# Kernel tuning notes

Hardware: AMD Instinct MI355X
Metric: run time of the kernel (lower is better)

## Reference

```python
import jax, jax.numpy as jnp
import numpy as np

B, N, F, K = 16384, 64, 128, 64


def setup_inputs() -> dict:
    key = jax.random.key(0)
    kx, kd = jax.random.split(key)
    x = jax.random.normal(kx, (B, F), dtype=jnp.float32)
    D = jax.random.normal(kd, (N, F, K), dtype=jnp.float32)  # per-cluster factor dictionaries
    return {"x": x, "D": D}


def reference(x, D):
    # --- assignment step (torch.no_grad in original) ---
    # Dtx[n,b,j] = sum_i D[n,i,j] * x[b,i]
    Dtx = jnp.einsum('nij,bi->nbj', D, x)                      # [N,B,K]
    # per-cluster (D^T D)^{-1}, batched inverse over the cluster axis
    DTD = jnp.einsum('nij,nik->njk', D, D)                     # [N,K,K]
    DTD_inv = jnp.linalg.inv(DTD)                              # [N,K,K]
    Cs = jnp.einsum('nbj,nkj->nbk', Dtx, DTD_inv)              # [N,B,K]
    x_hat = jnp.einsum('nij,nbj->nbi', D, Cs)                  # [N,B,F]
    # nearest-subspace assignment per sample
    label = jnp.argmin(jnp.linalg.norm(x_hat - x[None], axis=-1), axis=0)  # [B] int
    C = Cs[label, jnp.arange(x.shape[0])]                      # [B,K] gather per sample
    # --- reconstruction loss: sum_i || x[i] - D[label[i]] @ C[i] ||^2 ---
    x_rec = jnp.einsum('bik,bk->bi', D[label], C)              # grouped gather + matmul
    se_loss = jnp.sum(jnp.square(x - x_rec))
    return se_loss, label
```

## Files before the change

kernel.cpp:

```cpp
#include <hip/hip_runtime.h>
#include <hip/hip_bf16.h>

#define B_N 16384
#define TAU 0.25f
#define GS 68
#define YS 133

typedef float f32x4 __attribute__((ext_vector_type(4)));
typedef short s16x8 __attribute__((ext_vector_type(8)));

__device__ __forceinline__ void gl_lds16(const void* g, void* l) {
    __builtin_amdgcn_global_load_lds(
        (const __attribute__((address_space(1))) void*)g,
        (__attribute__((address_space(3))) void*)l, 16, 0, 0);
}

__device__ __forceinline__ unsigned short bf16_bits(float v) {
    __hip_bfloat16 h = __float2bfloat16(v);
    return *reinterpret_cast<unsigned short*>(&h);
}

__global__ __launch_bounds__(256) void prep_convert(const float* __restrict__ x,
                                                    const float* __restrict__ D,
                                                    unsigned short* __restrict__ xh,
                                                    float* __restrict__ nrm,
                                                    float* __restrict__ Qg,
                                                    unsigned short* __restrict__ Bht,
                                                    float* __restrict__ out) {
    const int t = threadIdx.x;

    if (blockIdx.x >= 64) {
        const int gid = (blockIdx.x - 64) * 256 + t;
        if (gid == 0) out[0] = 0.0f;
        const size_t base = (size_t)gid * 32;
        float s = 0.0f;
        #pragma unroll
        for (int c = 0; c < 8; ++c) {
            const f32x4 v = ((const f32x4*)(x + base))[c];
            s += v.x * v.x + v.y * v.y + v.z * v.z + v.w * v.w;
            ushort4 h;
            h.x = bf16_bits(v.x); h.y = bf16_bits(v.y);
            h.z = bf16_bits(v.z); h.w = bf16_bits(v.w);
            ((ushort4*)(xh + base))[c] = h;
        }
        s += __shfl_xor(s, 1, 64);
        s += __shfl_xor(s, 2, 64);
        if ((gid & 3) == 0) nrm[gid >> 2] = s;
        return;
    }

    __shared__ float Y[64 * YS];
    __shared__ __align__(16) float G[64 * GS + 64];
    __shared__ __align__(16) float Lti[8 * 8 * 8];
    const int n = blockIdx.x;
    const float* Dn = D + (size_t)n * 8192;

    for (int e4 = t; e4 < 2048; e4 += 256) {
        const int c = e4 >> 4, j4 = (e4 & 15) * 4;
        const f32x4 v = ((const f32x4*)Dn)[e4];
        Y[(j4 + 0) * YS + c] = v.x;
        Y[(j4 + 1) * YS + c] = v.y;
        Y[(j4 + 2) * YS + c] = v.z;
        Y[(j4 + 3) * YS + c] = v.w;
    }

    {
        const int a0 = (t & 15) * 4, b0 = (t >> 4) * 4;
        float acc[4][4] = {};
        #pragma unroll 4
        for (int i = 0; i < 128; ++i) {
            const f32x4 av = *(const f32x4*)(Dn + i * 64 + a0);
            const f32x4 bv = *(const f32x4*)(Dn + i * 64 + b0);
            const float aa[4] = {av.x, av.y, av.z, av.w};
            const float bb[4] = {bv.x, bv.y, bv.z, bv.w};
            #pragma unroll
            for (int p = 0; p < 4; ++p)
                #pragma unroll
                for (int q = 0; q < 4; ++q) acc[p][q] = fmaf(aa[p], bb[q], acc[p][q]);
        }
        #pragma unroll
        for (int p = 0; p < 4; ++p)
            #pragma unroll
            for (int q = 0; q < 4; ++q) G[(a0 + p) * GS + b0 + q] = acc[p][q];
    }
    __syncthreads();

    for (int p8 = 0; p8 < 8; ++p8) {
        const int pb = p8 * 8;
        if (t < 64) {
            const int lane = t;
            const f32x4 v0 = *(const f32x4*)&G[lane * GS + pb];
            const f32x4 v1 = *(const f32x4*)&G[lane * GS + pb + 4];
            float g[8] = {v0.x, v0.y, v0.z, v0.w, v1.x, v1.y, v1.z, v1.w};
            #pragma unroll
            for (int kk = 0; kk < 8; ++kk) {
                const int k = pb + kk;
                const float dk = __shfl(g[kk], k, 64);
                const float rinv = 1.0f / sqrtf(dk);
                const float lik = g[kk] * rinv;
                g[kk] = lik;
                if (lane == 0) G[64 * GS + k] = rinv;
                #pragma unroll
                for (int jj = kk + 1; jj < 8; ++jj) {
                    const float ljk = __shfl(lik, pb + jj, 64);
                    g[jj] -= lik * ljk;
                }
            }
            *(f32x4*)&G[lane * GS + pb]     = (f32x4){g[0], g[1], g[2], g[3]};
            *(f32x4*)&G[lane * GS + pb + 4] = (f32x4){g[4], g[5], g[6], g[7]};
        }
        __syncthreads();
        const int base = pb + 8;
        if (base < 64) {
            for (int i = base + (t >> 5); i < 64; i += 8) {
                const f32x4 Li0 = *(const f32x4*)&G[i * GS + pb];
                const f32x4 Li1 = *(const f32x4*)&G[i * GS + pb + 4];
                for (int j = base + (t & 31); j < 64; j += 32) {
                    const f32x4 Lj0 = *(const f32x4*)&G[j * GS + pb];
                    const f32x4 Lj1 = *(const f32x4*)&G[j * GS + pb + 4];
                    float s = G[i * GS + j];
                    s -= Li0.x * Lj0.x + Li0.y * Lj0.y + Li0.z * Lj0.z + Li0.w * Lj0.w;
                    s -= Li1.x * Lj1.x + Li1.y * Lj1.y + Li1.z * Lj1.z + Li1.w * Lj1.w;
                    G[i * GS + j] = s;
                }
            }
        }
        __syncthreads();
    }

    if (t < 64) {
        const int bi = t >> 3, c = t & 7;
        const int base = bi * 8;
        float m[8];
        #pragma unroll
        for (int r = 0; r < 8; ++r) {
            float s = (r == c) ? 1.0f : 0.0f;
            #pragma unroll
            for (int k = 0; k < r; ++k)
                s -= G[(base + r) * GS + base + k] * m[k];
            m[r] = s * G[64 * GS + base + r];
        }
        #pragma unroll
        for (int r = 0; r < 8; ++r) Lti[(base + r) * 8 + c] = m[r];
    }
    __syncthreads();

    if (t < 128) {
        const int c = t;
        for (int i = 0; i < 8; ++i) {
            float Tv[8];
            #pragma unroll
            for (int r = 0; r < 8; ++r) Tv[r] = Y[(i * 8 + r) * YS + c];
            for (int k = 0; k < i; ++k) {
                #pragma unroll
                for (int kk = 0; kk < 8; ++kk) {
                    const float z = Y[(k * 8 + kk) * YS + c];
                    #pragma unroll
                    for (int r = 0; r < 8; ++r)
                        Tv[r] -= G[(i * 8 + r) * GS + k * 8 + kk] * z;
                }
            }
            #pragma unroll
            for (int r = 0; r < 8; ++r) {
                float z = 0.0f;
                #pragma unroll
                for (int rp = 0; rp <= r; ++rp)
                    z += Lti[(i * 8 + r) * 8 + rp] * Tv[rp];
                Y[(i * 8 + r) * YS + c] = z;
            }
        }
    }
    __syncthreads();

    for (int e = t; e < 8192; e += 256) {
        const int j = e >> 7, i = e & 127;
        Bht[((size_t)n * 64 + j) * 128 + i] = bf16_bits(Y[j * YS + i]);
    }
    for (int e = t; e < 8192; e += 256) {
        const int i = e >> 6, j = e & 63;
        Qg[(size_t)n * 8192 + e] = Y[j * YS + i];
    }
}

__global__ __launch_bounds__(256) void gemm_scores(const unsigned short* __restrict__ xh,
                                                   const unsigned short* __restrict__ Bht,
                                                   float* __restrict__ S) {
    __shared__ unsigned short ldsA[128 * 128];
    __shared__ unsigned short ldsB[128 * 128];
    const int t = threadIdx.x, w = t >> 6, lane = t & 63;
    const int m0 = blockIdx.x * 128;
    const int nsplit = blockIdx.y;
    const int wm = w & 1, wn = w >> 1;

    {
        const int rl = lane >> 4;
        const int p  = lane & 15;
        #pragma unroll
        for (int q = 0; q < 8; ++q) {
            const int row = w * 32 + q * 4 + rl;
            const int c = p ^ (row & 15);
            gl_lds16(xh + (size_t)(m0 + row) * 128 + c * 8,
                     &ldsA[(w * 32 + q * 4) * 128]);
            gl_lds16(Bht + (size_t)(nsplit * 1024 + row) * 128 + c * 8,
                     &ldsB[(w * 32 + q * 4) * 128]);
        }
    }
    __syncthreads();

    s16x8 af[4][4];
    #pragma unroll
    for (int mt = 0; mt < 4; ++mt) {
        const int r = wm * 64 + mt * 16 + (lane & 15);
        #pragma unroll
        for (int ks = 0; ks < 4; ++ks) {
            const int p = (ks * 4 + (lane >> 4)) ^ (lane & 15);
            af[mt][ks] = *(const s16x8*)&ldsA[r * 128 + p * 8];
        }
    }

    #pragma unroll 1
    for (int it = 0; it < 8; ++it) {
        s16x8 bf[4][4];
        #pragma unroll
        for (int nt = 0; nt < 4; ++nt) {
            const int r = wn * 64 + nt * 16 + (lane & 15);
            #pragma unroll
            for (int ks = 0; ks < 4; ++ks) {
                const int p = (ks * 4 + (lane >> 4)) ^ (lane & 15);
                bf[nt][ks] = *(const s16x8*)&ldsB[r * 128 + p * 8];
            }
        }
        __syncthreads();

        if (it < 7) {
            const int rl = lane >> 4, p = lane & 15;
            #pragma unroll
            for (int q = 0; q < 8; ++q) {
                const int row = w * 32 + q * 4 + rl;
                const int c = p ^ (row & 15);
                gl_lds16(Bht + (size_t)(nsplit * 1024 + (it + 1) * 128 + row) * 128 + c * 8,
                         &ldsB[(w * 32 + q * 4) * 128]);
            }
        }

        const int nc = nsplit * 16 + it * 2 + wn;
        #pragma unroll
        for (int mt = 0; mt < 4; ++mt) {
            f32x4 acc[4];
            #pragma unroll
            for (int nt = 0; nt < 4; ++nt) acc[nt] = (f32x4){0.f, 0.f, 0.f, 0.f};
            #pragma unroll
            for (int ks = 0; ks < 4; ++ks)
                #pragma unroll
                for (int nt = 0; nt < 4; ++nt)
                    acc[nt] = __builtin_amdgcn_mfma_f32_16x16x32_bf16(
                        af[mt][ks], bf[nt][ks], acc[nt], 0, 0, 0);
            #pragma unroll
            for (int rg = 0; rg < 4; ++rg) {
                float p = 0.0f;
                #pragma unroll
                for (int nt = 0; nt < 4; ++nt) {
                    const float v = acc[nt][rg];
                    p += v * v;
                }
                p += __shfl_xor(p, 1, 64);
                p += __shfl_xor(p, 2, 64);
                p += __shfl_xor(p, 4, 64);
                p += __shfl_xor(p, 8, 64);
                if ((lane & 15) == 0) {
                    const int m = wm * 64 + mt * 16 + (lane >> 4) * 4 + rg;
                    S[(size_t)nc * B_N + m0 + m] = p;
                }
            }
        }
        __syncthreads();
    }
}

__global__ __launch_bounds__(256) void argmax_rescore(const float* __restrict__ Sa,
                                                      const float* __restrict__ nrm,
                                                      const float* __restrict__ x,
                                                      const float* __restrict__ Qg,
                                                      float* __restrict__ out) {
    __shared__ float tile[64 * 65];
    __shared__ int sflags[64];
    __shared__ int scnt;
    __shared__ float ssum;
    __shared__ float scorr[4];
    const int t = threadIdx.x, w = t >> 6, lane = t & 63;
    const int b0 = blockIdx.x * 64;
    if (t == 0) scnt = 0;

    for (int idx = t; idx < 1024; idx += 256) {
        const int n = idx >> 4, c4 = idx & 15;
        const f32x4 v = *(const f32x4*)&Sa[(size_t)n * B_N + b0 + c4 * 4];
        tile[(c4 * 4 + 0) * 65 + n] = v.x;
        tile[(c4 * 4 + 1) * 65 + n] = v.y;
        tile[(c4 * 4 + 2) * 65 + n] = v.z;
        tile[(c4 * 4 + 3) * 65 + n] = v.w;
    }
    __syncthreads();

    if (t < 64) {
        float v1 = -1e30f, v2 = -1e30f;
        int n1 = 0;
        for (int n = 0; n < 64; ++n) {
            const float v = tile[t * 65 + n];
            if (v > v1) { v2 = v1; v1 = v; n1 = n; }
            else v2 = fmaxf(v2, v);
        }
        out[1 + b0 + t] = (float)n1;
        if (v1 - v2 < TAU) { const int i = atomicAdd(&scnt, 1); sflags[i] = t; }
        float err = nrm[b0 + t] - v1;
        for (int off = 32; off; off >>= 1) err += __shfl_xor(err, off, 64);
        if (t == 0) ssum = err;
    }
    if (lane == 0) scorr[w] = 0.0f;
    __syncthreads();

    const int nf = scnt;
    float corr = 0.0f;
    for (int f = w; f < nf; f += 4) {
        const int s = sflags[f];
        const int b2 = b0 + s;
        const float v = tile[s * 65 + lane];
        float vm = v;
        for (int off = 32; off; off >>= 1) vm = fmaxf(vm, __shfl_xor(vm, off, 64));
        unsigned long long mask = __ballot((vm - v) < TAU);
        float best = -1e30f;
        int bn = 0;
        while (mask) {
            const int nn = (int)__builtin_ctzll(mask);
            mask &= mask - 1;
            const float* Qn = Qg + (size_t)nn * 8192;
            const float* xb = x + (size_t)b2 * 128;
            float d0 = 0.0f, d1 = 0.0f, d2 = 0.0f, d3 = 0.0f;
            #pragma unroll
            for (int i = 0; i < 128; i += 4) {
                d0 = fmaf(Qn[(i + 0) * 64 + lane], xb[i + 0], d0);
                d1 = fmaf(Qn[(i + 1) * 64 + lane], xb[i + 1], d1);
                d2 = fmaf(Qn[(i + 2) * 64 + lane], xb[i + 2], d2);
                d3 = fmaf(Qn[(i + 3) * 64 + lane], xb[i + 3], d3);
            }
            const float dot = (d0 + d1) + (d2 + d3);
            float sv = dot * dot;
            for (int off = 32; off; off >>= 1) sv += __shfl_xor(sv, off, 64);
            if (sv > best) { best = sv; bn = nn; }
        }
        if (lane == 0) {
            out[1 + b2] = (float)bn;
            corr += vm - best;
        }
    }
    if (lane == 0 && corr != 0.0f) scorr[w] += corr;
    __syncthreads();
    if (t == 0)
        atomicAdd(out, ssum + scorr[0] + scorr[1] + scorr[2] + scorr[3]);
}

extern "C" void kernel_launch(void* const* d_in, const int* in_sizes, int n_in,
                              void* d_out, int out_size, void* d_ws, size_t ws_size,
                              hipStream_t stream) {
    const float* x = (const float*)d_in[0];
    const float* D = (const float*)d_in[1];
    float* out = (float*)d_out;

    char* ws = (char*)d_ws;
    unsigned short* xh  = (unsigned short*)(ws);
    unsigned short* Bht = (unsigned short*)(ws + (4u << 20));
    float* Qg           = (float*)(ws + (5u << 20));
    float* Sa           = (float*)(ws + (7u << 20));
    float* nrm          = (float*)(ws + (11u << 20));

    prep_convert<<<320, 256, 0, stream>>>(x, D, xh, nrm, Qg, Bht, out);
    gemm_scores<<<dim3(128, 4), 256, 0, stream>>>(xh, Bht, Sa);
    argmax_rescore<<<256, 256, 0, stream>>>(Sa, nrm, x, Qg, out);
}
```

Measured before the change: 161.3 us.

## Fuse score GEMM with argmax and rescore, keeping scores in LDS

Merges the scoring GEMM and the argmax/rescore kernels into one kernel. Each block now covers 64 samples across all 64 clusters and keeps its score tile in shared memory that reuses the A/B staging space, so the global score array is no longer written and read back and one launch disappears. In exchange, the M tile shrinks from 128 to 64 rows and each block streams the whole Bht matrix. That halves reuse of B and roughly doubles L2 traffic for B, while the grid drops to 256 blocks.

```diff
diff --git a/kernel.cpp b/kernel.cpp
--- a/kernel.cpp
+++ b/kernel.cpp
@@ -182,70 +182,84 @@
     }
 }
 
-__global__ __launch_bounds__(256) void gemm_scores(const unsigned short* __restrict__ xh,
+__global__ __launch_bounds__(256) void gemm_argmax(const unsigned short* __restrict__ xh,
                                                    const unsigned short* __restrict__ Bht,
-                                                   float* __restrict__ S) {
-    __shared__ unsigned short ldsA[128 * 128];
-    __shared__ unsigned short ldsB[128 * 128];
+                                                   const float* __restrict__ nrm,
+                                                   const float* __restrict__ x,
+                                                   const float* __restrict__ Qg,
+                                                   float* __restrict__ out) {
+    __shared__ __align__(16) unsigned char lds_raw[49152];
+    unsigned short* ldsA = (unsigned short*)lds_raw;
+    unsigned short* ldsB = (unsigned short*)(lds_raw + 16384);
+    float* St = (float*)lds_raw;
+    __shared__ int sflags[64];
+    __shared__ int scnt;
+    __shared__ float ssum;
+    __shared__ float scorr[4];
+
     const int t = threadIdx.x, w = t >> 6, lane = t & 63;
-    const int m0 = blockIdx.x * 128;
-    const int nsplit = blockIdx.y;
+    const int b0 = blockIdx.x * 64;
     const int wm = w & 1, wn = w >> 1;
+    if (t == 0) scnt = 0;
 
     {
-        const int rl = lane >> 4;
-        const int p  = lane & 15;
+        const int rl = lane >> 4, p = lane & 15;
+        #pragma unroll
+        for (int q = 0; q < 4; ++q) {
+            const int row = w * 16 + q * 4 + rl;
+            const int c = p ^ (row & 15);
+            gl_lds16(xh + (size_t)(b0 + row) * 128 + c * 8,
+                     &ldsA[(w * 16 + q * 4) * 128]);
+        }
         #pragma unroll
         for (int q = 0; q < 8; ++q) {
             const int row = w * 32 + q * 4 + rl;
             const int c = p ^ (row & 15);
-            gl_lds16(xh + (size_t)(m0 + row) * 128 + c * 8,
-                     &ldsA[(w * 32 + q * 4) * 128]);
-            gl_lds16(Bht + (size_t)(nsplit * 1024 + row) * 128 + c * 8,
+            gl_lds16(Bht + (size_t)row * 128 + c * 8,
                      &ldsB[(w * 32 + q * 4) * 128]);
         }
     }
     __syncthreads();
 
-    s16x8 af[4][4];
+    s16x8 af[2][4];
     #pragma unroll
-    for (int mt = 0; mt < 4; ++mt) {
-        const int r = wm * 64 + mt * 16 + (lane & 15);
+    for (int mt = 0; mt < 2; ++mt) {
+        const int r = wm * 32 + mt * 16 + (lane & 15);
         #pragma unroll
         for (int ks = 0; ks < 4; ++ks) {
-            const int p = (ks * 4 + (lane >> 4)) ^ (lane & 15);
+            const int p = (ks * 4 + (lane >> 4)) ^ (r & 15);
             af[mt][ks] = *(const s16x8*)&ldsA[r * 128 + p * 8];
         }
     }
 
     #pragma unroll 1
-    for (int it = 0; it < 8; ++it) {
+    for (int it = 0; it < 32; ++it) {
         s16x8 bf[4][4];
         #pragma unroll
         for (int nt = 0; nt < 4; ++nt) {
             const int r = wn * 64 + nt * 16 + (lane & 15);
             #pragma unroll
             for (int ks = 0; ks < 4; ++ks) {
-                const int p = (ks * 4 + (lane >> 4)) ^ (lane & 15);
+                const int p = (ks * 4 + (lane >> 4)) ^ (r & 15);
                 bf[nt][ks] = *(const s16x8*)&ldsB[r * 128 + p * 8];
             }
         }
         __syncthreads();
 
-        if (it < 7) {
+        if (it < 31) {
             const int rl = lane >> 4, p = lane & 15;
             #pragma unroll
             for (int q = 0; q < 8; ++q) {
                 const int row = w * 32 + q * 4 + rl;
                 const int c = p ^ (row & 15);
-                gl_lds16(Bht + (size_t)(nsplit * 1024 + (it + 1) * 128 + row) * 128 + c * 8,
+                gl_lds16(Bht + (size_t)((it + 1) * 128 + row) * 128 + c * 8,
                          &ldsB[(w * 32 + q * 4) * 128]);
             }
         }
 
-        const int nc = nsplit * 16 + it * 2 + wn;
-        #pragma unroll
-        for (int mt = 0; mt < 4; ++mt) {
+        const int nc = it * 2 + wn;
+        #pragma unroll
+        for (int mt = 0; mt < 2; ++mt) {
             f32x4 acc[4];
             #pragma unroll
             for (int nt = 0; nt < 4; ++nt) acc[nt] = (f32x4){0.f, 0.f, 0.f, 0.f};
@@ -268,44 +282,19 @@
                 p += __shfl_xor(p, 4, 64);
                 p += __shfl_xor(p, 8, 64);
                 if ((lane & 15) == 0) {
-                    const int m = wm * 64 + mt * 16 + (lane >> 4) * 4 + rg;
-                    S[(size_t)nc * B_N + m0 + m] = p;
+                    const int m = wm * 32 + mt * 16 + (lane >> 4) * 4 + rg;
+                    St[nc * 64 + m] = p;
                 }
             }
         }
         __syncthreads();
     }
-}
-
-__global__ __launch_bounds__(256) void argmax_rescore(const float* __restrict__ Sa,
-                                                      const float* __restrict__ nrm,
-                                                      const float* __restrict__ x,
-                                                      const float* __restrict__ Qg,
-                                                      float* __restrict__ out) {
-    __shared__ float tile[64 * 65];
-    __shared__ int sflags[64];
-    __shared__ int scnt;
-    __shared__ float ssum;
-    __shared__ float scorr[4];
-    const int t = threadIdx.x, w = t >> 6, lane = t & 63;
-    const int b0 = blockIdx.x * 64;
-    if (t == 0) scnt = 0;
-
-    for (int idx = t; idx < 1024; idx += 256) {
-        const int n = idx >> 4, c4 = idx & 15;
-        const f32x4 v = *(const f32x4*)&Sa[(size_t)n * B_N + b0 + c4 * 4];
-        tile[(c4 * 4 + 0) * 65 + n] = v.x;
-        tile[(c4 * 4 + 1) * 65 + n] = v.y;
-        tile[(c4 * 4 + 2) * 65 + n] = v.z;
-        tile[(c4 * 4 + 3) * 65 + n] = v.w;
-    }
-    __syncthreads();
 
     if (t < 64) {
         float v1 = -1e30f, v2 = -1e30f;
         int n1 = 0;
         for (int n = 0; n < 64; ++n) {
-            const float v = tile[t * 65 + n];
+            const float v = St[n * 64 + t];
             if (v > v1) { v2 = v1; v1 = v; n1 = n; }
             else v2 = fmaxf(v2, v);
         }
@@ -323,7 +312,7 @@
     for (int f = w; f < nf; f += 4) {
         const int s = sflags[f];
         const int b2 = b0 + s;
-        const float v = tile[s * 65 + lane];
+        const float v = St[lane * 64 + s];
         float vm = v;
         for (int off = 32; off; off >>= 1) vm = fmaxf(vm, __shfl_xor(vm, off, 64));
         unsigned long long mask = __ballot((vm - v) < TAU);
@@ -369,10 +358,8 @@
     unsigned short* xh  = (unsigned short*)(ws);
     unsigned short* Bht = (unsigned short*)(ws + (4u << 20));
     float* Qg           = (float*)(ws + (5u << 20));
-    float* Sa           = (float*)(ws + (7u << 20));
     float* nrm          = (float*)(ws + (11u << 20));
 
     prep_convert<<<320, 256, 0, stream>>>(x, D, xh, nrm, Qg, Bht, out);
-    gemm_scores<<<dim3(128, 4), 256, 0, stream>>>(xh, Bht, Sa);
-    argmax_rescore<<<256, 256, 0, stream>>>(Sa, nrm, x, Qg, out);
-}
+    gemm_argmax<<<256, 256, 0, stream>>>(xh, Bht, nrm, x, Qg, out);
+}
```

Result: slower. 179.4 us (+11.3%).

## Fuse argmax/rescore into GEMM via last-block counter and double-buffer B tiles

Applied to the files above, without the earlier changes.

Merges the argmax/rescore kernel into the scoring GEMM. Each of the four column-split blocks for a row tile bumps an atomic counter, and the last one to finish does the argmax, flagging and rescoring for its 128 rows. The GEMM also loads A fragments straight from global memory into registers instead of staging them through LDS, and double-buffers the B tile so the prefetch overlaps the MFMA work. This removes one kernel launch and its inter-kernel gap, at the cost of more LDS per block, an atomic handshake with fences, and a serialized tail on the last-arriving block.

```diff
diff --git a/kernel.cpp b/kernel.cpp
--- a/kernel.cpp
+++ b/kernel.cpp
@@ -26,12 +26,14 @@
                                                     float* __restrict__ nrm,
                                                     float* __restrict__ Qg,
                                                     unsigned short* __restrict__ Bht,
+                                                    int* __restrict__ mcnt,
                                                     float* __restrict__ out) {
     const int t = threadIdx.x;
 
     if (blockIdx.x >= 64) {
         const int gid = (blockIdx.x - 64) * 256 + t;
         if (gid == 0) out[0] = 0.0f;
+        if (blockIdx.x == 64 && t < 128) mcnt[t] = 0;
         const size_t base = (size_t)gid * 32;
         float s = 0.0f;
         #pragma unroll
@@ -182,55 +184,54 @@
     }
 }
 
-__global__ __launch_bounds__(256) void gemm_scores(const unsigned short* __restrict__ xh,
-                                                   const unsigned short* __restrict__ Bht,
-                                                   float* __restrict__ S) {
-    __shared__ unsigned short ldsA[128 * 128];
-    __shared__ unsigned short ldsB[128 * 128];
+__global__ __launch_bounds__(256) void gemm_fused(
+        const unsigned short* __restrict__ xh,
+        const unsigned short* __restrict__ Bht,
+        float* __restrict__ Sa,
+        const float* __restrict__ nrm,
+        const float* __restrict__ x,
+        const float* __restrict__ Qg,
+        int* __restrict__ mcnt,
+        float* __restrict__ out) {
+    __shared__ __align__(16) unsigned char lraw[66560];
+    unsigned short* ldsB0 = (unsigned short*)lraw;
+    unsigned short* ldsB1 = (unsigned short*)(lraw + 32768);
+    float* St = (float*)lraw;
+    __shared__ int sflags[128];
+    __shared__ int scnt, lastFlag;
+    __shared__ float ssum[2];
+    __shared__ float scorr[4];
+
     const int t = threadIdx.x, w = t >> 6, lane = t & 63;
     const int m0 = blockIdx.x * 128;
     const int nsplit = blockIdx.y;
     const int wm = w & 1, wn = w >> 1;
+    const int lm = lane & 15, lg = lane >> 4;
+
+    s16x8 af[4][4];
+    #pragma unroll
+    for (int mt = 0; mt < 4; ++mt)
+        #pragma unroll
+        for (int ks = 0; ks < 4; ++ks)
+            af[mt][ks] = *(const s16x8*)(xh +
+                (size_t)(m0 + wm * 64 + mt * 16 + lm) * 128 + ks * 32 + lg * 8);
 
     {
-        const int rl = lane >> 4;
-        const int p  = lane & 15;
+        const int rl = lane >> 4, p = lane & 15;
         #pragma unroll
         for (int q = 0; q < 8; ++q) {
             const int row = w * 32 + q * 4 + rl;
             const int c = p ^ (row & 15);
-            gl_lds16(xh + (size_t)(m0 + row) * 128 + c * 8,
-                     &ldsA[(w * 32 + q * 4) * 128]);
             gl_lds16(Bht + (size_t)(nsplit * 1024 + row) * 128 + c * 8,
-                     &ldsB[(w * 32 + q * 4) * 128]);
-        }
-    }
-    __syncthreads();
-
-    s16x8 af[4][4];
-    #pragma unroll
-    for (int mt = 0; mt < 4; ++mt) {
-        const int r = wm * 64 + mt * 16 + (lane & 15);
-        #pragma unroll
-        for (int ks = 0; ks < 4; ++ks) {
-            const int p = (ks * 4 + (lane >> 4)) ^ (lane & 15);
-            af[mt][ks] = *(const s16x8*)&ldsA[r * 128 + p * 8];
-        }
-    }
+                     &ldsB0[(w * 32 + q * 4) * 128]);
+        }
+    }
+    __syncthreads();
 
     #pragma unroll 1
     for (int it = 0; it < 8; ++it) {
-        s16x8 bf[4][4];
-        #pragma unroll
-        for (int nt = 0; nt < 4; ++nt) {
-            const int r = wn * 64 + nt * 16 + (lane & 15);
-            #pragma unroll
-            for (int ks = 0; ks < 4; ++ks) {
-                const int p = (ks * 4 + (lane >> 4)) ^ (lane & 15);
-                bf[nt][ks] = *(const s16x8*)&ldsB[r * 128 + p * 8];
-            }
-        }
-        __syncthreads();
+        unsigned short* cur = (it & 1) ? ldsB1 : ldsB0;
+        unsigned short* nxt = (it & 1) ? ldsB0 : ldsB1;
 
         if (it < 7) {
             const int rl = lane >> 4, p = lane & 15;
@@ -239,7 +240,18 @@
                 const int row = w * 32 + q * 4 + rl;
                 const int c = p ^ (row & 15);
                 gl_lds16(Bht + (size_t)(nsplit * 1024 + (it + 1) * 128 + row) * 128 + c * 8,
-                         &ldsB[(w * 32 + q * 4) * 128]);
+                         &nxt[(w * 32 + q * 4) * 128]);
+            }
+        }
+
+        s16x8 bf[4][4];
+        #pragma unroll
+        for (int nt = 0; nt < 4; ++nt) {
+            const int r = wn * 64 + nt * 16 + lm;
+            #pragma unroll
+            for (int ks = 0; ks < 4; ++ks) {
+                const int p = (ks * 4 + lg) ^ (r & 15);
+                bf[nt][ks] = *(const s16x8*)&cur[r * 128 + p * 8];
             }
         }
 
@@ -267,53 +279,43 @@
                 p += __shfl_xor(p, 2, 64);
                 p += __shfl_xor(p, 4, 64);
                 p += __shfl_xor(p, 8, 64);
-                if ((lane & 15) == 0) {
-                    const int m = wm * 64 + mt * 16 + (lane >> 4) * 4 + rg;
-                    S[(size_t)nc * B_N + m0 + m] = p;
-                }
+                if (lm == 0)
+                    Sa[(size_t)nc * B_N + m0 + wm * 64 + mt * 16 + lg * 4 + rg] = p;
             }
         }
         __syncthreads();
     }
-}
-
-__global__ __launch_bounds__(256) void argmax_rescore(const float* __restrict__ Sa,
-                                                      const float* __restrict__ nrm,
-                                                      const float* __restrict__ x,
-                                                      const float* __restrict__ Qg,
-                                                      float* __restrict__ out) {
-    __shared__ float tile[64 * 65];
-    __shared__ int sflags[64];
-    __shared__ int scnt;
-    __shared__ float ssum;
-    __shared__ float scorr[4];
-    const int t = threadIdx.x, w = t >> 6, lane = t & 63;
-    const int b0 = blockIdx.x * 64;
-    if (t == 0) scnt = 0;
-
-    for (int idx = t; idx < 1024; idx += 256) {
-        const int n = idx >> 4, c4 = idx & 15;
-        const f32x4 v = *(const f32x4*)&Sa[(size_t)n * B_N + b0 + c4 * 4];
-        tile[(c4 * 4 + 0) * 65 + n] = v.x;
-        tile[(c4 * 4 + 1) * 65 + n] = v.y;
-        tile[(c4 * 4 + 2) * 65 + n] = v.z;
-        tile[(c4 * 4 + 3) * 65 + n] = v.w;
-    }
-    __syncthreads();
-
-    if (t < 64) {
+
+    __threadfence();
+    if (t == 0) {
+        const int old = __hip_atomic_fetch_add(&mcnt[blockIdx.x], 1,
+                            __ATOMIC_ACQ_REL, __HIP_MEMORY_SCOPE_AGENT);
+        lastFlag = (old == 3) ? 1 : 0;
+        scnt = 0;
+    }
+    __syncthreads();
+    if (!lastFlag) return;
+    __threadfence();
+
+    for (int e = t; e < 8192; e += 256) {
+        const int n = e >> 7, m = e & 127;
+        St[m * 69 + n] = Sa[(size_t)n * B_N + m0 + m];
+    }
+    __syncthreads();
+
+    if (t < 128) {
         float v1 = -1e30f, v2 = -1e30f;
         int n1 = 0;
         for (int n = 0; n < 64; ++n) {
-            const float v = tile[t * 65 + n];
+            const float v = St[t * 69 + n];
             if (v > v1) { v2 = v1; v1 = v; n1 = n; }
             else v2 = fmaxf(v2, v);
         }
-        out[1 + b0 + t] = (float)n1;
+        out[1 + m0 + t] = (float)n1;
         if (v1 - v2 < TAU) { const int i = atomicAdd(&scnt, 1); sflags[i] = t; }
-        float err = nrm[b0 + t] - v1;
+        float err = nrm[m0 + t] - v1;
         for (int off = 32; off; off >>= 1) err += __shfl_xor(err, off, 64);
-        if (t == 0) ssum = err;
+        if (lane == 0) ssum[w] = err;
     }
     if (lane == 0) scorr[w] = 0.0f;
     __syncthreads();
@@ -322,8 +324,8 @@
     float corr = 0.0f;
     for (int f = w; f < nf; f += 4) {
         const int s = sflags[f];
-        const int b2 = b0 + s;
-        const float v = tile[s * 65 + lane];
+        const int b2 = m0 + s;
+        const float v = St[s * 69 + lane];
         float vm = v;
         for (int off = 32; off; off >>= 1) vm = fmaxf(vm, __shfl_xor(vm, off, 64));
         unsigned long long mask = __ballot((vm - v) < TAU);
@@ -355,7 +357,7 @@
     if (lane == 0 && corr != 0.0f) scorr[w] += corr;
     __syncthreads();
     if (t == 0)
-        atomicAdd(out, ssum + scorr[0] + scorr[1] + scorr[2] + scorr[3]);
+        atomicAdd(out, ssum[0] + ssum[1] + scorr[0] + scorr[1] + scorr[2] + scorr[3]);
 }
 
 extern "C" void kernel_launch(void* const* d_in, const int* in_sizes, int n_in,
@@ -371,8 +373,8 @@
     float* Qg           = (float*)(ws + (5u << 20));
     float* Sa           = (float*)(ws + (7u << 20));
     float* nrm          = (float*)(ws + (11u << 20));
-
-    prep_convert<<<320, 256, 0, stream>>>(x, D, xh, nrm, Qg, Bht, out);
-    gemm_scores<<<dim3(128, 4), 256, 0, stream>>>(xh, Bht, Sa);
-    argmax_rescore<<<256, 256, 0, stream>>>(Sa, nrm, x, Qg, out);
-}
+    int* mcnt           = (int*)(ws + (11u << 20) + 65536);
+
+    prep_convert<<<320, 256, 0, stream>>>(x, D, xh, nrm, Qg, Bht, mcnt, out);
+    gemm_fused<<<dim3(128, 4), 256, 0, stream>>>(xh, Bht, Sa, nrm, x, Qg, mcnt, out);
+}
```

Result: slower. 212.6 us (+31.9%).

## Double grid size for score GEMM and argmax kernels with smaller per-block tiles

Applied to the files above, without the earlier changes.

The score GEMM now gives each block 8 clusters (64 columns per step) instead of 16, and the four waves split the 128 rows instead of a 2x2 wave grid. This doubles the grid to 1024 blocks and halves the B-tile LDS footprint, which should improve occupancy and load balance on the many CUs. The argmax/rescore kernel also halves its tile to 32 samples per block, doubling that grid. The cost is less B-fragment reuse per A load and more blocks, so global traffic and the per-block overhead go up.

```diff
diff --git a/kernel.cpp b/kernel.cpp
--- a/kernel.cpp
+++ b/kernel.cpp
@@ -186,47 +186,53 @@
                                                    const unsigned short* __restrict__ Bht,
                                                    float* __restrict__ S) {
     __shared__ unsigned short ldsA[128 * 128];
-    __shared__ unsigned short ldsB[128 * 128];
+    __shared__ unsigned short ldsB[64 * 128];
     const int t = threadIdx.x, w = t >> 6, lane = t & 63;
     const int m0 = blockIdx.x * 128;
-    const int nsplit = blockIdx.y;
-    const int wm = w & 1, wn = w >> 1;
+    const int n0 = blockIdx.y * 8;
+    const int lm = lane & 15, lg = lane >> 4;
 
     {
-        const int rl = lane >> 4;
-        const int p  = lane & 15;
+        const int rl = lane >> 4, p = lane & 15;
         #pragma unroll
         for (int q = 0; q < 8; ++q) {
             const int row = w * 32 + q * 4 + rl;
             const int c = p ^ (row & 15);
             gl_lds16(xh + (size_t)(m0 + row) * 128 + c * 8,
                      &ldsA[(w * 32 + q * 4) * 128]);
-            gl_lds16(Bht + (size_t)(nsplit * 1024 + row) * 128 + c * 8,
-                     &ldsB[(w * 32 + q * 4) * 128]);
-        }
-    }
-    __syncthreads();
-
-    s16x8 af[4][4];
+        }
+        #pragma unroll
+        for (int q = 0; q < 4; ++q) {
+            const int row = w * 16 + q * 4 + rl;
+            const int c = p ^ (row & 15);
+            gl_lds16(Bht + ((size_t)n0 * 64 + row) * 128 + c * 8,
+                     &ldsB[(w * 16 + q * 4) * 128]);
+        }
+    }
+    __syncthreads();
+
+    s16x8 af[2][4];
     #pragma unroll
-    for (int mt = 0; mt < 4; ++mt) {
-        const int r = wm * 64 + mt * 16 + (lane & 15);
+    for (int mt = 0; mt < 2; ++mt) {
+        const int r = w * 32 + mt * 16 + lm;
         #pragma unroll
         for (int ks = 0; ks < 4; ++ks) {
-            const int p = (ks * 4 + (lane >> 4)) ^ (lane & 15);
+            const int p = (ks * 4 + lg) ^ (r & 15);
             af[mt][ks] = *(const s16x8*)&ldsA[r * 128 + p * 8];
         }
     }
 
     #pragma unroll 1
     for (int it = 0; it < 8; ++it) {
+        const int nc = n0 + it;
+
         s16x8 bf[4][4];
         #pragma unroll
         for (int nt = 0; nt < 4; ++nt) {
-            const int r = wn * 64 + nt * 16 + (lane & 15);
+            const int r = nt * 16 + lm;
             #pragma unroll
             for (int ks = 0; ks < 4; ++ks) {
-                const int p = (ks * 4 + (lane >> 4)) ^ (lane & 15);
+                const int p = (ks * 4 + lg) ^ (r & 15);
                 bf[nt][ks] = *(const s16x8*)&ldsB[r * 128 + p * 8];
             }
         }
@@ -235,17 +241,16 @@
         if (it < 7) {
             const int rl = lane >> 4, p = lane & 15;
             #pragma unroll
-            for (int q = 0; q < 8; ++q) {
-                const int row = w * 32 + q * 4 + rl;
+            for (int q = 0; q < 4; ++q) {
+                const int row = w * 16 + q * 4 + rl;
                 const int c = p ^ (row & 15);
-                gl_lds16(Bht + (size_t)(nsplit * 1024 + (it + 1) * 128 + row) * 128 + c * 8,
-                         &ldsB[(w * 32 + q * 4) * 128]);
-            }
-        }
-
-        const int nc = nsplit * 16 + it * 2 + wn;
-        #pragma unroll
-        for (int mt = 0; mt < 4; ++mt) {
+                gl_lds16(Bht + ((size_t)(nc + 1) * 64 + row) * 128 + c * 8,
+                         &ldsB[(w * 16 + q * 4) * 128]);
+            }
+        }
+
+        #pragma unroll
+        for (int mt = 0; mt < 2; ++mt) {
             f32x4 acc[4];
             #pragma unroll
             for (int nt = 0; nt < 4; ++nt) acc[nt] = (f32x4){0.f, 0.f, 0.f, 0.f};
@@ -267,10 +272,8 @@
                 p += __shfl_xor(p, 2, 64);
                 p += __shfl_xor(p, 4, 64);
                 p += __shfl_xor(p, 8, 64);
-                if ((lane & 15) == 0) {
-                    const int m = wm * 64 + mt * 16 + (lane >> 4) * 4 + rg;
-                    S[(size_t)nc * B_N + m0 + m] = p;
-                }
+                if (lm == 0)
+                    S[(size_t)nc * B_N + m0 + w * 32 + mt * 16 + lg * 4 + rg] = p;
             }
         }
         __syncthreads();
@@ -282,17 +285,17 @@
                                                       const float* __restrict__ x,
                                                       const float* __restrict__ Qg,
                                                       float* __restrict__ out) {
-    __shared__ float tile[64 * 65];
-    __shared__ int sflags[64];
+    __shared__ float tile[32 * 65];
+    __shared__ int sflags[32];
     __shared__ int scnt;
     __shared__ float ssum;
     __shared__ float scorr[4];
     const int t = threadIdx.x, w = t >> 6, lane = t & 63;
-    const int b0 = blockIdx.x * 64;
+    const int b0 = blockIdx.x * 32;
     if (t == 0) scnt = 0;
 
-    for (int idx = t; idx < 1024; idx += 256) {
-        const int n = idx >> 4, c4 = idx & 15;
+    for (int e = t; e < 512; e += 256) {
+        const int n = e >> 3, c4 = e & 7;
         const f32x4 v = *(const f32x4*)&Sa[(size_t)n * B_N + b0 + c4 * 4];
         tile[(c4 * 4 + 0) * 65 + n] = v.x;
         tile[(c4 * 4 + 1) * 65 + n] = v.y;
@@ -301,7 +304,7 @@
     }
     __syncthreads();
 
-    if (t < 64) {
+    if (t < 32) {
         float v1 = -1e30f, v2 = -1e30f;
         int n1 = 0;
         for (int n = 0; n < 64; ++n) {
@@ -312,7 +315,11 @@
         out[1 + b0 + t] = (float)n1;
         if (v1 - v2 < TAU) { const int i = atomicAdd(&scnt, 1); sflags[i] = t; }
         float err = nrm[b0 + t] - v1;
-        for (int off = 32; off; off >>= 1) err += __shfl_xor(err, off, 64);
+        err += __shfl_xor(err, 1, 64);
+        err += __shfl_xor(err, 2, 64);
+        err += __shfl_xor(err, 4, 64);
+        err += __shfl_xor(err, 8, 64);
+        err += __shfl_xor(err, 16, 64);
         if (t == 0) ssum = err;
     }
     if (lane == 0) scorr[w] = 0.0f;
@@ -373,6 +380,6 @@
     float* nrm          = (float*)(ws + (11u << 20));
 
     prep_convert<<<320, 256, 0, stream>>>(x, D, xh, nrm, Qg, Bht, out);
-    gemm_scores<<<dim3(128, 4), 256, 0, stream>>>(xh, Bht, Sa);
-    argmax_rescore<<<256, 256, 0, stream>>>(Sa, nrm, x, Qg, out);
-}
+    gemm_scores<<<dim3(128, 8), 256, 0, stream>>>(xh, Bht, Sa);
+    argmax_rescore<<<512, 256, 0, stream>>>(Sa, nrm, x, Qg, out);
+}
```

Measured after the change: 159.4 us. About the same (-1.1%).
